# Kernel tuning notes

Measured on AMD Instinct MI355X. Metric: run time of the kernel, lower is better.

## Reference

```python
import jax, jax.numpy as jnp
import numpy as np

REVIEW_RATIO = 0.3  # init kwarg


def setup_inputs() -> dict:
    key = jax.random.key(0)
    k1, k2 = jax.random.split(key)
    N, C = 32768, 1000
    output = jax.random.normal(k1, (N, C), dtype=jnp.float32)
    target = jax.random.randint(k2, (N,), 0, C, dtype=jnp.int64)
    return {"output": output, "target": target}


def reference(output, target):
    # per-sample cross-entropy: -log_softmax(output)[i, target[i]]
    logp = jax.nn.log_softmax(output, axis=-1)               # [N, C]
    ce = -jnp.take_along_axis(logp, target[:, None], axis=-1)[:, 0]  # [N]
    n = ce.shape[0]
    k = int(n * REVIEW_RATIO)
    # descending sort; threshold is the k-th largest loss
    sorted_desc = jnp.sort(ce)[::-1]
    lam = sorted_desc[k]
    # zero out losses strictly below the threshold, then mean over ALL samples
    kept = jnp.where(ce < lam, jnp.zeros_like(ce), ce)
    return kept.mean()
```

## Files before the change

### kernel.cpp

```cpp
#include <hip/hip_runtime.h>
#include <stdint.h>


typedef unsigned int uint32;
typedef float vfloat4 __attribute__((ext_vector_type(4)));

#define LDNT(p) __builtin_nontemporal_load(p)

__device__ __forceinline__ float reduce_ce(vfloat4 v0, vfloat4 v1, vfloat4 v2,
                                           vfloat4 v3, float ot) {
  float m = fmaxf(fmaxf(fmaxf(v0.x, v0.y), fmaxf(v0.z, v0.w)),
                  fmaxf(fmaxf(fmaxf(v1.x, v1.y), fmaxf(v1.z, v1.w)),
                        fmaxf(fmaxf(fmaxf(v2.x, v2.y), fmaxf(v2.z, v2.w)),
                              fmaxf(fmaxf(v3.x, v3.y), fmaxf(v3.z, v3.w)))));
#pragma unroll
  for (int off = 1; off < 64; off <<= 1) m = fmaxf(m, __shfl_xor(m, off));
  float e = __expf(v0.x - m) + __expf(v0.y - m) + __expf(v0.z - m) + __expf(v0.w - m)
          + __expf(v1.x - m) + __expf(v1.y - m) + __expf(v1.z - m) + __expf(v1.w - m)
          + __expf(v2.x - m) + __expf(v2.y - m) + __expf(v2.z - m) + __expf(v2.w - m)
          + __expf(v3.x - m) + __expf(v3.y - m) + __expf(v3.z - m) + __expf(v3.w - m);
#pragma unroll
  for (int off = 1; off < 64; off <<= 1) e += __shfl_xor(e, off);
  return fmaxf((m - ot) + __logf(e), 0.0f);
}

__device__ __forceinline__ float extract_elem(vfloat4 v0, vfloat4 v1,
                                              vfloat4 v2, vfloat4 v3, int t) {
  const int q = t >> 2;
  const int comp = t & 3;
  const int set = q >> 6;
  const int src = q & 63;
  vfloat4 v = (set == 0) ? v0 : (set == 1) ? v1 : (set == 2) ? v2 : v3;
  float val = (comp == 0) ? v.x : (comp == 1) ? v.y : (comp == 2) ? v.z : v.w;
  return __shfl(val, src);
}

__global__ __launch_bounds__(256) void ce_kernel(
    const float* __restrict__ logits, const int* __restrict__ target,
    float* __restrict__ ce, int N, int C) {
  const int lane = (int)(threadIdx.x & 63);
  const int wave = (int)((blockIdx.x * blockDim.x + threadIdx.x) >> 6);
  const int r0 = wave * 4;
  if (r0 >= N) return;

  const int nv4 = C >> 2;
  const vfloat4 NEG = {-INFINITY, -INFINITY, -INFINITY, -INFINITY};
  const vfloat4* p0 = (const vfloat4*)(logits + (size_t)r0 * (size_t)C);

  const bool has1 = (r0 + 1 < N);
  const bool has2 = (r0 + 2 < N);
  const bool has3 = (r0 + 3 < N);

  const int t0 = target[r0];
  const int t1 = has1 ? target[r0 + 1] : 0;
  const int t2 = has2 ? target[r0 + 2] : 0;
  const int t3 = has3 ? target[r0 + 3] : 0;

#define LOADQ(d0, d1, d2, d3, bp)                          \
  d0 = (lane       < nv4) ? LDNT((bp) + lane      ) : NEG; \
  d1 = (lane +  64 < nv4) ? LDNT((bp) + lane +  64) : NEG; \
  d2 = (lane + 128 < nv4) ? LDNT((bp) + lane + 128) : NEG; \
  d3 = (lane + 192 < nv4) ? LDNT((bp) + lane + 192) : NEG;

  vfloat4 a0, a1, a2, a3, b0, b1, b2, b3;
  const vfloat4* p1 = p0 + nv4;
  const vfloat4* p2 = p1 + nv4;
  const vfloat4* p3 = p2 + nv4;

  LOADQ(a0, a1, a2, a3, p0);

  if (has1) { LOADQ(b0, b1, b2, b3, p1); }
  {
    float ot = extract_elem(a0, a1, a2, a3, t0);
    float cev = reduce_ce(a0, a1, a2, a3, ot);
    if (lane == 0) ce[r0] = cev;
  }
  if (!has1) return;

  if (has2) { LOADQ(a0, a1, a2, a3, p2); }
  {
    float ot = extract_elem(b0, b1, b2, b3, t1);
    float cev = reduce_ce(b0, b1, b2, b3, ot);
    if (lane == 0) ce[r0 + 1] = cev;
  }
  if (!has2) return;

  if (has3) { LOADQ(b0, b1, b2, b3, p3); }
  {
    float ot = extract_elem(a0, a1, a2, a3, t2);
    float cev = reduce_ce(a0, a1, a2, a3, ot);
    if (lane == 0) ce[r0 + 2] = cev;
  }
  if (!has3) return;

  {
    float ot = extract_elem(b0, b1, b2, b3, t3);
    float cev = reduce_ce(b0, b1, b2, b3, ot);
    if (lane == 0) ce[r0 + 3] = cev;
  }
#undef LOADQ
}


__device__ void find_level_1024(uint32* H, uint32* g, uint32 rank, int tid,
                                volatile uint32* sel) {
  uint32 c = 0;
#pragma unroll
  for (int j = 0; j < 8; ++j) {
    uint32 w = H[8 * tid + j];
    c += (w & 0xFFFFu) + (w >> 16);
  }
  g[tid] = c;
  __syncthreads();
  for (int off = 1; off < 1024; off <<= 1) {
    uint32 v = g[tid] + ((tid + off < 1024) ? g[tid + off] : 0u);
    __syncthreads();
    g[tid] = v;
    __syncthreads();
  }
  uint32 SG = (tid + 1 < 1024) ? g[tid + 1] : 0u;
  if (SG <= rank && rank < g[tid]) { sel[0] = (uint32)tid; sel[1] = rank - SG; }
  __syncthreads();
  if (tid == 0) {
    uint32 grp = sel[0], kg = sel[1], acc = 0;
    for (int b = 15; b >= 0; --b) {
      uint32 bin = grp * 16u + (uint32)b;
      uint32 w = H[bin >> 1];
      uint32 cc = (bin & 1u) ? (w >> 16) : (w & 0xFFFFu);
      if (kg < acc + cc) { sel[0] = bin; sel[1] = kg - acc; break; }
      acc += cc;
    }
  }
  __syncthreads();
}

__global__ __launch_bounds__(1024) void select_kernel(
    const float* __restrict__ ce, float* __restrict__ out, int N, int k) {
  __shared__ uint32 H[8192];
  __shared__ uint32 Cand[8192];
  __shared__ uint32 g[1024];
  __shared__ uint32 sel[2];
  __shared__ uint32 ccnt;
  __shared__ uint32 cnt8[8];
  __shared__ double wsum[16];
  const int tid = (int)threadIdx.x;
  const int lane = tid & 63;
  const float4* ce4 = (const float4*)ce;
  const int N4 = N >> 2;

  if (tid == 0) ccnt = 0;
  if (tid < 8) cnt8[tid] = 0;
  for (int j = tid; j < 8192; j += 1024) H[j] = 0;
  __syncthreads();

  for (int i = tid; i < N4; i += 1024) {
    float4 x = ce4[i];
    uint32 k0 = __float_as_uint(x.x) >> 17;
    uint32 k1 = __float_as_uint(x.y) >> 17;
    uint32 k2 = __float_as_uint(x.z) >> 17;
    uint32 k3 = __float_as_uint(x.w) >> 17;
    atomicAdd(&H[k0 >> 1], (k0 & 1u) ? 0x10000u : 1u);
    atomicAdd(&H[k1 >> 1], (k1 & 1u) ? 0x10000u : 1u);
    atomicAdd(&H[k2 >> 1], (k2 & 1u) ? 0x10000u : 1u);
    atomicAdd(&H[k3 >> 1], (k3 & 1u) ? 0x10000u : 1u);
  }
  __syncthreads();
  find_level_1024(H, g, (uint32)k, tid, sel);
  const uint32 K = sel[0];
  const uint32 kr1 = sel[1];
  __syncthreads();

  double acc = 0.0;
  const int iters = (N4 + 1023) / 1024;
  for (int it = 0; it < iters; ++it) {
    int i = it * 1024 + tid;
    bool valid = (i < N4);
    float4 x = make_float4(0.f, 0.f, 0.f, 0.f);
    if (valid) x = ce4[i];
    float f[4] = {x.x, x.y, x.z, x.w};
#pragma unroll
    for (int j = 0; j < 4; ++j) {
      uint32 u = __float_as_uint(f[j]);
      uint32 key = u >> 17;
      if (valid && key > K) acc += (double)f[j];
      bool mine = valid && (key == K);
      unsigned long long mk = __ballot(mine);
      if (mk) {
        int src = (int)__ffsll(mk) - 1;
        uint32 base = 0;
        if (lane == src) base = atomicAdd(&ccnt, (uint32)__popcll(mk));
        base = (uint32)__shfl((int)base, src);
        if (mine) {
          uint32 p = base + (uint32)__popcll(mk & ((1ull << lane) - 1ull));
          if (p < 8192u) Cand[p] = u;
        }
      }
    }
  }
  __syncthreads();
  const uint32 c = (ccnt < 8192u) ? ccnt : 8192u;

  for (int j = tid; j < 8192; j += 1024) H[j] = 0;
  __syncthreads();
  for (uint32 j = (uint32)tid; j < c; j += 1024u) {
    uint32 k2 = (Cand[j] >> 3) & 0x3FFFu;
    atomicAdd(&H[k2 >> 1], (k2 & 1u) ? 0x10000u : 1u);
  }
  __syncthreads();
  find_level_1024(H, g, kr1, tid, sel);
  const uint32 B2 = sel[0];
  const uint32 kr2 = sel[1];
  __syncthreads();

  const uint32 lam_hi = (K << 17) | (B2 << 3);

  for (uint32 j = (uint32)tid; j < c; j += 1024u) {
    uint32 u = Cand[j];
    if ((u >> 3) == (lam_hi >> 3)) atomicAdd(&cnt8[u & 7u], 1u);
  }
  __syncthreads();
  if (tid == 0) {
    uint32 kg = kr2, a2 = 0;
    for (int b = 7; b >= 0; --b) {
      uint32 cc = cnt8[b];
      if (kg < a2 + cc) { sel[0] = lam_hi | (uint32)b; break; }
      a2 += cc;
    }
  }
  __syncthreads();
  const uint32 lam = sel[0];

  for (uint32 j = (uint32)tid; j < c; j += 1024u) {
    uint32 u = Cand[j];
    if (u >= lam) acc += (double)__uint_as_float(u);
  }

#pragma unroll
  for (int off = 1; off < 64; off <<= 1) acc += __shfl_xor(acc, off);
  if ((tid & 63) == 0) wsum[tid >> 6] = acc;
  __syncthreads();
  if (tid == 0) {
    double tsum = 0.0;
    for (int i = 0; i < 16; ++i) tsum += wsum[i];
    out[0] = (float)(tsum / (double)N);
  }
}

extern "C" void kernel_launch(void* const* d_in, const int* in_sizes, int n_in,
                              void* d_out, int out_size, void* d_ws, size_t ws_size,
                              hipStream_t stream) {
  const float* logits = (const float*)d_in[0];
  const int* target = (const int*)d_in[1];
  float* out = (float*)d_out;

  const int N = in_sizes[1];
  const int C = in_sizes[0] / N;
  const int k = (int)((double)N * 0.3);

  float* ce = (float*)d_ws;

  int nblk = (N + 15) / 16;
  ce_kernel<<<nblk, 256, 0, stream>>>(logits, target, ce, N, C);

  select_kernel<<<1, 1024, 0, stream>>>(ce, out, N, k);
}
```

Before: 196.2 us.

## Fuse CE and top-k selection into one kernel with last-block finalization

Merges the cross-entropy kernel and the single-block selection kernel into one launch. Each block now writes per-row losses and also adds them into a global histogram through atomics, and the last block to finish (found with a done counter) runs the selection. This removes the second kernel launch and the single block's first histogram pass over all N losses. In exchange it adds a memset launch, a global atomic per row, and 1024-thread blocks for the CE phase, which may lower occupancy.

```diff
diff --git a/kernel.cpp b/kernel.cpp
--- a/kernel.cpp
+++ b/kernel.cpp
@@ -35,73 +35,6 @@
   return __shfl(val, src);
 }
 
-__global__ __launch_bounds__(256) void ce_kernel(
-    const float* __restrict__ logits, const int* __restrict__ target,
-    float* __restrict__ ce, int N, int C) {
-  const int lane = (int)(threadIdx.x & 63);
-  const int wave = (int)((blockIdx.x * blockDim.x + threadIdx.x) >> 6);
-  const int r0 = wave * 4;
-  if (r0 >= N) return;
-
-  const int nv4 = C >> 2;
-  const vfloat4 NEG = {-INFINITY, -INFINITY, -INFINITY, -INFINITY};
-  const vfloat4* p0 = (const vfloat4*)(logits + (size_t)r0 * (size_t)C);
-
-  const bool has1 = (r0 + 1 < N);
-  const bool has2 = (r0 + 2 < N);
-  const bool has3 = (r0 + 3 < N);
-
-  const int t0 = target[r0];
-  const int t1 = has1 ? target[r0 + 1] : 0;
-  const int t2 = has2 ? target[r0 + 2] : 0;
-  const int t3 = has3 ? target[r0 + 3] : 0;
-
-#define LOADQ(d0, d1, d2, d3, bp)                          \
-  d0 = (lane       < nv4) ? LDNT((bp) + lane      ) : NEG; \
-  d1 = (lane +  64 < nv4) ? LDNT((bp) + lane +  64) : NEG; \
-  d2 = (lane + 128 < nv4) ? LDNT((bp) + lane + 128) : NEG; \
-  d3 = (lane + 192 < nv4) ? LDNT((bp) + lane + 192) : NEG;
-
-  vfloat4 a0, a1, a2, a3, b0, b1, b2, b3;
-  const vfloat4* p1 = p0 + nv4;
-  const vfloat4* p2 = p1 + nv4;
-  const vfloat4* p3 = p2 + nv4;
-
-  LOADQ(a0, a1, a2, a3, p0);
-
-  if (has1) { LOADQ(b0, b1, b2, b3, p1); }
-  {
-    float ot = extract_elem(a0, a1, a2, a3, t0);
-    float cev = reduce_ce(a0, a1, a2, a3, ot);
-    if (lane == 0) ce[r0] = cev;
-  }
-  if (!has1) return;
-
-  if (has2) { LOADQ(a0, a1, a2, a3, p2); }
-  {
-    float ot = extract_elem(b0, b1, b2, b3, t1);
-    float cev = reduce_ce(b0, b1, b2, b3, ot);
-    if (lane == 0) ce[r0 + 1] = cev;
-  }
-  if (!has2) return;
-
-  if (has3) { LOADQ(b0, b1, b2, b3, p3); }
-  {
-    float ot = extract_elem(a0, a1, a2, a3, t2);
-    float cev = reduce_ce(a0, a1, a2, a3, ot);
-    if (lane == 0) ce[r0 + 2] = cev;
-  }
-  if (!has3) return;
-
-  {
-    float ot = extract_elem(b0, b1, b2, b3, t3);
-    float cev = reduce_ce(b0, b1, b2, b3, ot);
-    if (lane == 0) ce[r0 + 3] = cev;
-  }
-#undef LOADQ
-}
-
-
 __device__ void find_level_1024(uint32* H, uint32* g, uint32 rank, int tid,
                                 volatile uint32* sel) {
   uint32 c = 0;
@@ -134,8 +67,11 @@
   __syncthreads();
 }
 
-__global__ __launch_bounds__(1024) void select_kernel(
-    const float* __restrict__ ce, float* __restrict__ out, int N, int k) {
+__global__ __launch_bounds__(1024) void fused_kernel(
+    const float* __restrict__ logits, const int* __restrict__ target,
+    float* __restrict__ ce, uint32* __restrict__ hist,
+    uint32* __restrict__ done, float* __restrict__ out,
+    int N, int C, int k) {
   __shared__ uint32 H[8192];
   __shared__ uint32 Cand[8192];
   __shared__ uint32 g[1024];
@@ -143,28 +79,101 @@
   __shared__ uint32 ccnt;
   __shared__ uint32 cnt8[8];
   __shared__ double wsum[16];
+  __shared__ int s_last;
+
   const int tid = (int)threadIdx.x;
   const int lane = tid & 63;
+
+  {
+    const int wave = (int)((blockIdx.x * blockDim.x + threadIdx.x) >> 6);
+    const int r0 = wave * 4;
+    if (r0 < N) {
+      const int nv4 = C >> 2;
+      const vfloat4 NEG = {-INFINITY, -INFINITY, -INFINITY, -INFINITY};
+      const vfloat4* p0 = (const vfloat4*)(logits + (size_t)r0 * (size_t)C);
+
+      const bool has1 = (r0 + 1 < N);
+      const bool has2 = (r0 + 2 < N);
+      const bool has3 = (r0 + 3 < N);
+
+      const int t0 = target[r0];
+      const int t1 = has1 ? target[r0 + 1] : 0;
+      const int t2 = has2 ? target[r0 + 2] : 0;
+      const int t3 = has3 ? target[r0 + 3] : 0;
+
+#define LOADQ(d0, d1, d2, d3, bp)                          \
+  d0 = (lane       < nv4) ? LDNT((bp) + lane      ) : NEG; \
+  d1 = (lane +  64 < nv4) ? LDNT((bp) + lane +  64) : NEG; \
+  d2 = (lane + 128 < nv4) ? LDNT((bp) + lane + 128) : NEG; \
+  d3 = (lane + 192 < nv4) ? LDNT((bp) + lane + 192) : NEG;
+
+#define EMIT(row, cev)                                                    \
+  if (lane == 0) {                                                        \
+    ce[row] = (cev);                                                      \
+    atomicAdd(&hist[__float_as_uint(cev) >> 17], 1u);                     \
+  }
+
+      vfloat4 a0, a1, a2, a3, b0, b1, b2, b3;
+      const vfloat4* p1 = p0 + nv4;
+      const vfloat4* p2 = p1 + nv4;
+      const vfloat4* p3 = p2 + nv4;
+
+      LOADQ(a0, a1, a2, a3, p0);
+
+      if (has1) { LOADQ(b0, b1, b2, b3, p1); }
+      {
+        float ot = extract_elem(a0, a1, a2, a3, t0);
+        float cev = reduce_ce(a0, a1, a2, a3, ot);
+        EMIT(r0, cev);
+      }
+      if (has1) {
+        if (has2) { LOADQ(a0, a1, a2, a3, p2); }
+        {
+          float ot = extract_elem(b0, b1, b2, b3, t1);
+          float cev = reduce_ce(b0, b1, b2, b3, ot);
+          EMIT(r0 + 1, cev);
+        }
+        if (has2) {
+          if (has3) { LOADQ(b0, b1, b2, b3, p3); }
+          {
+            float ot = extract_elem(a0, a1, a2, a3, t2);
+            float cev = reduce_ce(a0, a1, a2, a3, ot);
+            EMIT(r0 + 2, cev);
+          }
+          if (has3) {
+            float ot = extract_elem(b0, b1, b2, b3, t3);
+            float cev = reduce_ce(b0, b1, b2, b3, ot);
+            EMIT(r0 + 3, cev);
+          }
+        }
+      }
+#undef LOADQ
+#undef EMIT
+    }
+  }
+
+  __syncthreads();
+  if (tid == 0) {
+    __threadfence();
+    s_last = (atomicAdd(done, 1u) == (uint32)(gridDim.x - 1)) ? 1 : 0;
+  }
+  __syncthreads();
+  if (!s_last) return;
+  __threadfence();
+
   const float4* ce4 = (const float4*)ce;
   const int N4 = N >> 2;
 
+#pragma unroll
+  for (int j = 0; j < 8; ++j) {
+    uint32 lo = hist[16 * tid + 2 * j];
+    uint32 hi = hist[16 * tid + 2 * j + 1];
+    H[8 * tid + j] = (lo & 0xFFFFu) | (hi << 16);
+  }
   if (tid == 0) ccnt = 0;
   if (tid < 8) cnt8[tid] = 0;
-  for (int j = tid; j < 8192; j += 1024) H[j] = 0;
-  __syncthreads();
-
-  for (int i = tid; i < N4; i += 1024) {
-    float4 x = ce4[i];
-    uint32 k0 = __float_as_uint(x.x) >> 17;
-    uint32 k1 = __float_as_uint(x.y) >> 17;
-    uint32 k2 = __float_as_uint(x.z) >> 17;
-    uint32 k3 = __float_as_uint(x.w) >> 17;
-    atomicAdd(&H[k0 >> 1], (k0 & 1u) ? 0x10000u : 1u);
-    atomicAdd(&H[k1 >> 1], (k1 & 1u) ? 0x10000u : 1u);
-    atomicAdd(&H[k2 >> 1], (k2 & 1u) ? 0x10000u : 1u);
-    atomicAdd(&H[k3 >> 1], (k3 & 1u) ? 0x10000u : 1u);
-  }
-  __syncthreads();
+  __syncthreads();
+
   find_level_1024(H, g, (uint32)k, tid, sel);
   const uint32 K = sel[0];
   const uint32 kr1 = sel[1];
@@ -258,9 +267,12 @@
   const int k = (int)((double)N * 0.3);
 
   float* ce = (float*)d_ws;
-
-  int nblk = (N + 15) / 16;
-  ce_kernel<<<nblk, 256, 0, stream>>>(logits, target, ce, N, C);
-
-  select_kernel<<<1, 1024, 0, stream>>>(ce, out, N, k);
-}
+  uint32* hist = (uint32*)((char*)d_ws + (size_t)N * sizeof(float));
+  uint32* done = hist + 16384;
+
+  hipMemsetAsync(hist, 0, 16384 * sizeof(uint32) + sizeof(uint32), stream);
+
+  int nblk = (N + 63) / 64;
+  fused_kernel<<<nblk, 1024, 0, stream>>>(logits, target, ce, hist, done, out,
+                                          N, C, k);
+}
```

Result: slower. 339.4 us (+73.0%).
